# Optimization experiments

Hardware: AMD Instinct MI355X
Metric: run time of the kernel (lower is better)

Reference implementation:

```python
import jax, jax.numpy as jnp
import numpy as np

THRESHOLD = 0.003  # pool_type[3]
EPS = 1e-7


def setup_inputs() -> dict:
    key = jax.random.key(0)
    k1, k2, k3, k4 = jax.random.split(key, 4)
    B, N, C = 64, 600, 256
    x = jax.random.normal(k1, (B, N, C), dtype=jnp.float32)
    A = jax.random.uniform(k2, (B, N, N), dtype=jnp.float32)
    mask = jax.random.bernoulli(k3, 0.9, (B, N))
    # small-scale projection weight so exp(scores) stays well-conditioned
    W = jax.random.normal(k4, (1, C), dtype=jnp.float32) * 0.05
    return {"x": x, "A": A, "mask": mask, "W": W}


def reference(x, A, mask, W):
    B, N, C = x.shape
    mf = mask.astype(x.dtype)
    # proj(x) -> (B,N,1) -> (B,N); alpha_pre = exp(.) masked
    scores = jnp.einsum('bnc,oc->bn', x, W)
    alpha_pre = jnp.exp(scores) * mf
    alpha = alpha_pre / (jnp.sum(alpha_pre, axis=1, keepdims=True) + EPS)
    x = x * alpha[..., None]
    # threshold masking
    mask = mask & (alpha > THRESHOLD)
    # drop_nodes_edges: topk over mask values + gather-compaction of x and A.
    # Static K=N (JIT-safe); equivalent to torch's dynamic N_nodes_max up to
    # trailing zero padding (padded rows/cols are fully masked out below).
    mvals, idx = jax.lax.top_k(mask.astype(jnp.int32), N)  # (B,N)
    mask_k = mvals.astype(bool)
    x = jnp.take_along_axis(x, idx[..., None], axis=1)          # (B,N,C)
    A = jnp.take_along_axis(A, idx[..., None], axis=1)          # rows
    A = jnp.take_along_axis(A, idx[:, None, :], axis=2)         # cols
    mask_matrix = mask_k[:, :, None] & mask_k[:, None, :]
    A = A * mask_matrix.astype(A.dtype)
    return x, A, mask_k
```

## Files before the change

### kernel.cpp

```cpp
#include <hip/hip_runtime.h>

#define B_DIM 64
#define N_NODES 600
#define C_DIM 256
#define NV4 (N_NODES / 4)
#define XROWS (B_DIM * N_NODES)
#define XBLOCKS (XROWS / 4)
#define A_ROWTILE 16
#define ABLK_PER_B ((N_NODES + A_ROWTILE - 1) / A_ROWTILE)
#define ABLOCKS (B_DIM * ABLK_PER_B)

constexpr float kThr = 0.003f;
constexpr float kEps = 1e-7f;

__global__ __launch_bounds__(256)
void k_scores(const float* __restrict__ x,
              const float* __restrict__ W,
              const int* __restrict__ mask,
              float* __restrict__ alpha_pre) {
  const int row  = blockIdx.x * 4 + (threadIdx.x >> 6);
  const int lane = threadIdx.x & 63;
  const float4 xv = reinterpret_cast<const float4*>(x + (size_t)row * C_DIM)[lane];
  const float4 wv = reinterpret_cast<const float4*>(W)[lane];
  float s = xv.x * wv.x + xv.y * wv.y + xv.z * wv.z + xv.w * wv.w;
  #pragma unroll
  for (int off = 32; off > 0; off >>= 1) s += __shfl_down(s, off, 64);
  if (lane == 0) {
    alpha_pre[row] = (mask[row] != 0) ? expf(s) : 0.0f;
  }
}

__global__ __launch_bounds__(1024)
void k_compact(float* __restrict__ alpha,
               int* __restrict__ idx,
               int* __restrict__ Kbuf,
               float* __restrict__ mask_out) {
  const int b    = blockIdx.x;
  const int t    = threadIdx.x;
  const int wave = t >> 6;
  const int lane = t & 63;

  __shared__ float fs[1024];
  __shared__ int   wtot[16];

  const float ap = (t < N_NODES) ? alpha[b * N_NODES + t] : 0.0f;

  fs[t] = ap;
  __syncthreads();
  #pragma unroll
  for (int off = 512; off > 0; off >>= 1) {
    if (t < off) fs[t] += fs[t + off];
    __syncthreads();
  }
  const float S = fs[0];

  const float a = ap / (S + kEps);
  const int keep = (t < N_NODES && a > kThr) ? 1 : 0;

  int incl = keep;
  #pragma unroll
  for (int off = 1; off < 64; off <<= 1) {
    int v = __shfl_up(incl, off, 64);
    if (lane >= off) incl += v;
  }
  if (lane == 63) wtot[wave] = incl;
  __syncthreads();
  int offtot = 0, Ktot = 0;
  #pragma unroll
  for (int w2 = 0; w2 < 16; ++w2) {
    const int v = wtot[w2];
    if (w2 < wave) offtot += v;
    Ktot += v;
  }
  incl += offtot;
  const int K = Ktot;

  if (t < N_NODES) {
    const int pos = keep ? (incl - 1) : (K + (t - incl));
    idx[b * N_NODES + pos]    = t;
    alpha[b * N_NODES + t]    = a;
    mask_out[b * N_NODES + t] = (t < K) ? 1.0f : 0.0f;
    if (t == 0) Kbuf[b] = K;
  }
}

__global__ __launch_bounds__(256)
void k_gather(const float* __restrict__ x,
              const float* __restrict__ A,
              const float* __restrict__ alpha,
              const int* __restrict__ idx,
              const int* __restrict__ Kbuf,
              float* __restrict__ xo,
              float* __restrict__ Ao) {
  const int bid  = blockIdx.x;
  const int t    = threadIdx.x;
  const int wave = t >> 6;
  const int lane = t & 63;

  if (bid < XBLOCKS) {
    const int row = bid * 4 + wave;
    const int b   = row / N_NODES;
    const int src = idx[row];
    const float a = alpha[b * N_NODES + src];
    float4 v = reinterpret_cast<const float4*>(
        x + ((size_t)b * N_NODES + src) * C_DIM)[lane];
    v.x *= a; v.y *= a; v.z *= a; v.w *= a;
    reinterpret_cast<float4*>(xo + (size_t)row * C_DIM)[lane] = v;
  } else {
    const int abid = bid - XBLOCKS;
    const int b    = abid / ABLK_PER_B;
    const int i0   = (abid % ABLK_PER_B) * A_ROWTILE;

    __shared__ int sidx[N_NODES];
    const int K = Kbuf[b];
    for (int j = t; j < K; j += 256) sidx[j] = idx[b * N_NODES + j];
    __syncthreads();

    const float* Ab  = A  + (size_t)b * N_NODES * N_NODES;
    float*       Aob = Ao + (size_t)b * N_NODES * N_NODES;

    for (int ii = wave; ii < A_ROWTILE; ii += 4) {
      const int i = i0 + ii;
      if (i >= N_NODES) break;
      float4* orow = reinterpret_cast<float4*>(Aob + (size_t)i * N_NODES);
      if (i < K) {
        const float* Arow = Ab + (size_t)sidx[i] * N_NODES;
        for (int j4 = lane; j4 < NV4; j4 += 64) {
          const int j = j4 * 4;
          float4 v;
          v.x = (j + 0 < K) ? Arow[sidx[j + 0]] : 0.0f;
          v.y = (j + 1 < K) ? Arow[sidx[j + 1]] : 0.0f;
          v.z = (j + 2 < K) ? Arow[sidx[j + 2]] : 0.0f;
          v.w = (j + 3 < K) ? Arow[sidx[j + 3]] : 0.0f;
          orow[j4] = v;
        }
      } else {
        const float4 z = {0.0f, 0.0f, 0.0f, 0.0f};
        for (int j4 = lane; j4 < NV4; j4 += 64) orow[j4] = z;
      }
    }
  }
}

extern "C" void kernel_launch(void* const* d_in, const int* in_sizes, int n_in,
                              void* d_out, int out_size, void* d_ws, size_t ws_size,
                              hipStream_t stream) {
  const float* x    = (const float*)d_in[0];
  const float* A    = (const float*)d_in[1];
  const int*   mask = (const int*)d_in[2];
  const float* W    = (const float*)d_in[3];

  const size_t BN = (size_t)B_DIM * N_NODES;

  float* xo = (float*)d_out;
  float* Ao = xo + BN * C_DIM;
  float* mo = Ao + BN * N_NODES;

  float* alpha = (float*)d_ws;
  int*   idx   = (int*)(alpha + BN);
  int*   Kbuf  = idx + BN;

  k_scores<<<XBLOCKS, 256, 0, stream>>>(x, W, mask, alpha);
  k_compact<<<B_DIM, 1024, 0, stream>>>(alpha, idx, Kbuf, mo);
  k_gather<<<XBLOCKS + ABLOCKS, 256, 0, stream>>>(x, A, alpha, idx, Kbuf, xo, Ao);
}
```

Baseline: 43.91 us.

## Zero A output in scores kernel and restrict gather to the kept KxK block

The zero-fill of the compacted adjacency output moves into the first kernel, run by extra blocks alongside the score computation. The gather kernel now exits early for row tiles at or beyond K and writes only the columns up to K in kept rows. The idea is to take the bulk zero stores off the critical path after compaction and overlap them with the score pass's reads of x. Total bytes written stay about the same, and the output ends up depending on writes from two different kernels.

New measurement: 44.69 us. No clear change (+1.8%).

```diff
diff --git a/kernel.cpp b/kernel.cpp
--- a/kernel.cpp
+++ b/kernel.cpp
@@ -6,6 +6,11 @@
 #define NV4 (N_NODES / 4)
 #define XROWS (B_DIM * N_NODES)
 #define XBLOCKS (XROWS / 4)
+
+#define AO_F4 (B_DIM * N_NODES * NV4)
+#define ZBLOCKS 1440
+#define ZCHUNK (AO_F4 / ZBLOCKS)
+
 #define A_ROWTILE 16
 #define ABLK_PER_B ((N_NODES + A_ROWTILE - 1) / A_ROWTILE)
 #define ABLOCKS (B_DIM * ABLK_PER_B)
@@ -14,19 +19,28 @@
 constexpr float kEps = 1e-7f;
 
 __global__ __launch_bounds__(256)
-void k_scores(const float* __restrict__ x,
-              const float* __restrict__ W,
-              const int* __restrict__ mask,
-              float* __restrict__ alpha_pre) {
-  const int row  = blockIdx.x * 4 + (threadIdx.x >> 6);
-  const int lane = threadIdx.x & 63;
-  const float4 xv = reinterpret_cast<const float4*>(x + (size_t)row * C_DIM)[lane];
-  const float4 wv = reinterpret_cast<const float4*>(W)[lane];
-  float s = xv.x * wv.x + xv.y * wv.y + xv.z * wv.z + xv.w * wv.w;
-  #pragma unroll
-  for (int off = 32; off > 0; off >>= 1) s += __shfl_down(s, off, 64);
-  if (lane == 0) {
-    alpha_pre[row] = (mask[row] != 0) ? expf(s) : 0.0f;
+void k_scores_zero(const float* __restrict__ x,
+                   const float* __restrict__ W,
+                   const int* __restrict__ mask,
+                   float* __restrict__ alpha_pre,
+                   float4* __restrict__ Ao4) {
+  const int bid = blockIdx.x;
+  if (bid < XBLOCKS) {
+    const int row  = bid * 4 + (threadIdx.x >> 6);
+    const int lane = threadIdx.x & 63;
+    const float4 xv = reinterpret_cast<const float4*>(x + (size_t)row * C_DIM)[lane];
+    const float4 wv = reinterpret_cast<const float4*>(W)[lane];
+    float s = xv.x * wv.x + xv.y * wv.y + xv.z * wv.z + xv.w * wv.w;
+    #pragma unroll
+    for (int off = 32; off > 0; off >>= 1) s += __shfl_down(s, off, 64);
+    if (lane == 0) {
+      alpha_pre[row] = (mask[row] != 0) ? expf(s) : 0.0f;
+    }
+  } else {
+    const int zb = bid - XBLOCKS;
+    float4* dst = Ao4 + (size_t)zb * ZCHUNK;
+    const float4 z = {0.0f, 0.0f, 0.0f, 0.0f};
+    for (int i = threadIdx.x; i < ZCHUNK; i += 256) dst[i] = z;
   }
 }
 
@@ -111,32 +125,37 @@
     const int b    = abid / ABLK_PER_B;
     const int i0   = (abid % ABLK_PER_B) * A_ROWTILE;
 
+    const int K = Kbuf[b];
+    if (i0 >= K) return;
+
     __shared__ int sidx[N_NODES];
-    const int K = Kbuf[b];
     for (int j = t; j < K; j += 256) sidx[j] = idx[b * N_NODES + j];
     __syncthreads();
 
+    const int kq = K >> 2;
     const float* Ab  = A  + (size_t)b * N_NODES * N_NODES;
     float*       Aob = Ao + (size_t)b * N_NODES * N_NODES;
 
     for (int ii = wave; ii < A_ROWTILE; ii += 4) {
       const int i = i0 + ii;
-      if (i >= N_NODES) break;
+      if (i >= K) break;
       float4* orow = reinterpret_cast<float4*>(Aob + (size_t)i * N_NODES);
-      if (i < K) {
-        const float* Arow = Ab + (size_t)sidx[i] * N_NODES;
-        for (int j4 = lane; j4 < NV4; j4 += 64) {
+      const float* Arow = Ab + (size_t)sidx[i] * N_NODES;
+      for (int j4 = lane; j4 <= kq && j4 < NV4; j4 += 64) {
+        float4 v = {0.0f, 0.0f, 0.0f, 0.0f};
+        if (j4 < kq) {
           const int j = j4 * 4;
-          float4 v;
-          v.x = (j + 0 < K) ? Arow[sidx[j + 0]] : 0.0f;
-          v.y = (j + 1 < K) ? Arow[sidx[j + 1]] : 0.0f;
-          v.z = (j + 2 < K) ? Arow[sidx[j + 2]] : 0.0f;
-          v.w = (j + 3 < K) ? Arow[sidx[j + 3]] : 0.0f;
-          orow[j4] = v;
+          v.x = Arow[sidx[j + 0]];
+          v.y = Arow[sidx[j + 1]];
+          v.z = Arow[sidx[j + 2]];
+          v.w = Arow[sidx[j + 3]];
+        } else {
+          const int j = j4 * 4;
+          if (j + 0 < K) v.x = Arow[sidx[j + 0]];
+          if (j + 1 < K) v.y = Arow[sidx[j + 1]];
+          if (j + 2 < K) v.z = Arow[sidx[j + 2]];
         }
-      } else {
-        const float4 z = {0.0f, 0.0f, 0.0f, 0.0f};
-        for (int j4 = lane; j4 < NV4; j4 += 64) orow[j4] = z;
+        orow[j4] = v;
       }
     }
   }
@@ -160,7 +179,8 @@
   int*   idx   = (int*)(alpha + BN);
   int*   Kbuf  = idx + BN;
 
-  k_scores<<<XBLOCKS, 256, 0, stream>>>(x, W, mask, alpha);
+  k_scores_zero<<<XBLOCKS + ZBLOCKS, 256, 0, stream>>>(
+      x, W, mask, alpha, (float4*)Ao);
   k_compact<<<B_DIM, 1024, 0, stream>>>(alpha, idx, Kbuf, mo);
   k_gather<<<XBLOCKS + ABLOCKS, 256, 0, stream>>>(x, A, alpha, idx, Kbuf, xo, Ao);
 }
```
